# Optimization experiments

Measured on AMD Instinct MI355X. Metric: run time of the kernel, lower is better.

## Reference

```python
import jax, jax.numpy as jnp
import numpy as np
import math

B, T, D = 4, 4096, 1024
H, M = 16, 64
Dh = D // H


def _rope_tables(head_dim, max_seq_len, base=10000):
    inv_freq = 1.0 / (base ** (np.arange(0, head_dim, 2, dtype=np.float32) / head_dim))
    t = np.arange(max_seq_len, dtype=np.float32)
    freqs = np.einsum('i,j->ij', t, inv_freq)  # [T, Dh/2]
    cos = np.cos(freqs)
    sin = np.sin(freqs)
    # interleave (c, c) pairwise -> [T, Dh]
    cos = np.stack((cos, cos), axis=-1).reshape(max_seq_len, head_dim)
    sin = np.stack((sin, sin), axis=-1).reshape(max_seq_len, head_dim)
    return jnp.asarray(cos), jnp.asarray(sin)


def setup_inputs() -> dict:
    key = jax.random.key(0)
    ks = jax.random.split(key, 6)
    s = 1.0 / math.sqrt(D)
    x = jax.random.normal(ks[0], (B, T, D), dtype=jnp.float32)
    Wq = jnp.clip(jax.random.normal(ks[1], (D, D)) * s, -2 * s, 2 * s).astype(jnp.float32)
    Wk = jnp.clip(jax.random.normal(ks[2], (D, D)) * s, -2 * s, 2 * s).astype(jnp.float32)
    Wv = jnp.clip(jax.random.normal(ks[3], (D, D)) * s, -2 * s, 2 * s).astype(jnp.float32)
    Wo = jnp.clip(jax.random.normal(ks[4], (D, D)) * s, -2 * s, 2 * s).astype(jnp.float32)
    latent_code = (jax.random.normal(ks[5], (H, M, Dh)) * 0.02).astype(jnp.float32)
    rope_cos, rope_sin = _rope_tables(Dh, T)
    mask = jnp.ones((B, 1, T, 1), dtype=jnp.int32)
    return {'x': x, 'Wq': Wq, 'Wk': Wk, 'Wv': Wv, 'Wo': Wo,
            'latent_code': latent_code, 'rope_cos': rope_cos,
            'rope_sin': rope_sin, 'mask': mask}


def _rotate(x):
    # (x1, x2) pairs -> (-x2, x1), interleaved
    x2 = x.reshape(*x.shape[:-1], -1, 2)
    return jnp.stack((-x2[..., 1], x2[..., 0]), axis=-1).reshape(x.shape)


def reference(x, Wq, Wk, Wv, Wo, latent_code, rope_cos, rope_sin, mask):
    Bc, Tc, Dc = x.shape
    scale = 1.0 / math.sqrt(Dh)
    # projections -> [B, H, T, Dh]
    q = (x @ Wq.T).reshape(Bc, Tc, H, Dh).transpose(0, 2, 1, 3)
    k = (x @ Wk.T).reshape(Bc, Tc, H, Dh).transpose(0, 2, 1, 3)
    v = (x @ Wv.T).reshape(Bc, Tc, H, Dh).transpose(0, 2, 1, 3)
    cos = rope_cos[:Tc][None, None]  # [1,1,T,Dh]
    sin = rope_sin[:Tc][None, None]
    q = q * cos + _rotate(q) * sin
    k = k * cos + _rotate(k) * sin
    # Stage 1: token -> latent assignment, softmax over tokens (axis=2)
    assign_logits = jnp.einsum('bhtd,hmd->bhtm', k, latent_code) * scale
    assign_logits = jnp.where(mask == 0, -jnp.inf, assign_logits)
    assign = jax.nn.softmax(assign_logits, axis=2)
    k_lat = jnp.einsum('bhtm,bhtd->bhmd', assign, k)
    v_lat = jnp.einsum('bhtm,bhtd->bhmd', assign, v)
    # Stage 2: query attends to latents, softmax over latents (axis=-1)
    att2 = jnp.einsum('bhtd,bhmd->bhtm', q, k_lat) * scale
    p2 = jax.nn.softmax(att2, axis=-1)
    out = jnp.einsum('bhtm,bhmd->bhtd', p2, v_lat)
    out = out.transpose(0, 2, 1, 3).reshape(Bc, Tc, Dc)
    return out @ Wo.T
```

## Files before the change

### kernel.cpp

```cpp
#include <hip/hip_runtime.h>
#include <hip/hip_bf16.h>
#include <stdint.h>


#define DEV static __device__ __forceinline__

using short8 = __attribute__((ext_vector_type(8))) short;
using f32x4  = __attribute__((ext_vector_type(4))) float;

#define ZERO4 (f32x4){0.f, 0.f, 0.f, 0.f}

DEV float bf2f(unsigned short u) {
  union { unsigned int i; float f; } c; c.i = ((unsigned int)u) << 16; return c.f;
}
DEV unsigned short f2bf(float f) {
  __hip_bfloat16 h = __float2bfloat16(f);
  unsigned short u; __builtin_memcpy(&u, &h, 2); return u;
}
DEV f32x4 mfma16(short8 a, short8 b, f32x4 c) {
  return __builtin_amdgcn_mfma_f32_16x16x32_bf16(a, b, c, 0, 0, 0);
}
#define GLOAD_LDS16(G, L) __builtin_amdgcn_global_load_lds( \
    (const __attribute__((address_space(1))) void*)(G),     \
    (__attribute__((address_space(3))) void*)(L), 16, 0, 0)

__global__ void cvt_all(const float* __restrict__ x,
                        const float* __restrict__ Wq, const float* __restrict__ Wk,
                        const float* __restrict__ Wv, const float* __restrict__ Wo,
                        __hip_bfloat16* __restrict__ xb,
                        __hip_bfloat16* __restrict__ Wb) {
  const int bid = blockIdx.x;
  const float* src;
  __hip_bfloat16* dst;
  int base;
  if (bid < 16384) {
    src = x; dst = xb; base = bid;
  } else {
    const int k = (bid - 16384) >> 10;
    src = (k == 0) ? Wq : (k == 1) ? Wk : (k == 2) ? Wv : Wo;
    dst = Wb + (size_t)k * 1048576;
    base = (bid - 16384) & 1023;
  }
  const int i = (base * 256 + threadIdx.x) * 4;
  const float4 v = *(const float4*)(src + i);
  ushort4 o;
  o.x = f2bf(v.x); o.y = f2bf(v.y); o.z = f2bf(v.z); o.w = f2bf(v.w);
  *(ushort4*)(dst + i) = o;
}

template<int MODE, int ROPE>
__global__ __launch_bounds__(512, 2)
void gemm256(const __hip_bfloat16* __restrict__ A,
             const __hip_bfloat16* __restrict__ Bt,
             void* __restrict__ Cout, __hip_bfloat16* __restrict__ Ct,
             const float* __restrict__ cosT, const float* __restrict__ sinT,
             int M, int N, int K) {
  __shared__ __hip_bfloat16 As[2][256 * 64];
  __shared__ __hip_bfloat16 Bs[2][256 * 64];
  const int tid = threadIdx.x;
  const int w = tid >> 6, l = tid & 63;
  const int lr = l & 15, lg = l >> 4;
  const int rowA0 = blockIdx.x * 256;
  const int colB0 = blockIdx.y * 256;
  const int srow = w * 8 + (l >> 3);
  const int skk  = (((l & 7) ^ (l >> 3)) * 8);
  const __hip_bfloat16* Ab = A  + (size_t)(rowA0 + srow) * K + skk;
  const __hip_bfloat16* Bb = Bt + (size_t)(colB0 + srow) * K + skk;
  f32x4 acc[8][4];
#pragma unroll
  for (int i = 0; i < 8; ++i)
#pragma unroll
    for (int j = 0; j < 4; ++j) acc[i][j] = ZERO4;
  const int wr = (w >> 2) * 128;
  const int wc = (w & 3) * 64;
  const int NT = K >> 6;

#define G_STAGE(kt, buf)                                                          \
  {                                                                               \
    const int k0s = (kt) * 64;                                                    \
    _Pragma("unroll")                                                             \
    for (int i = 0; i < 4; ++i) {                                                 \
      GLOAD_LDS16(Ab + (size_t)(i * 64) * K + k0s, &As[buf][i * 4096 + w * 512]); \
      GLOAD_LDS16(Bb + (size_t)(i * 64) * K + k0s, &Bs[buf][i * 4096 + w * 512]); \
    }                                                                             \
  }

  G_STAGE(0, 0);
  for (int kt = 0; kt < NT; ++kt) {
    const int cur = kt & 1;
    if (kt + 1 < NT) {
      G_STAGE(kt + 1, cur ^ 1);
      asm volatile("s_waitcnt vmcnt(8)" ::: "memory");
    } else {
      asm volatile("s_waitcnt vmcnt(0)" ::: "memory");
    }
    __builtin_amdgcn_s_barrier();
    __builtin_amdgcn_s_setprio(1);
#pragma unroll
    for (int s = 0; s < 2; ++s) {
      short8 fa[8], fb[4];
#pragma unroll
      for (int i = 0; i < 8; ++i)
        fa[i] = *(const short8*)&As[cur][(wr + i * 16 + lr) * 64 +
                                         (((s * 4 + lg) ^ (lr & 7)) * 8)];
#pragma unroll
      for (int j = 0; j < 4; ++j)
        fb[j] = *(const short8*)&Bs[cur][(wc + j * 16 + lr) * 64 +
                                         (((s * 4 + lg) ^ (lr & 7)) * 8)];
#pragma unroll
      for (int i = 0; i < 8; ++i)
#pragma unroll
        for (int j = 0; j < 4; ++j)
          acc[i][j] = mfma16(fa[i], fb[j], acc[i][j]);
    }
    __builtin_amdgcn_s_setprio(0);
    __builtin_amdgcn_s_barrier();
  }
#undef G_STAGE

  const int r0 = rowA0 + wr + lg * 4;
  const int c0 = colB0 + wc + lr;
  if (ROPE) {
#pragma unroll
    for (int i = 0; i < 8; ++i)
#pragma unroll
      for (int j = 0; j < 4; ++j)
#pragma unroll
        for (int r = 0; r < 4; ++r) {
          const int m = r0 + i * 16 + r;
          const int n = c0 + j * 16;
          const int t = m & 4095, d = n & 63;
          const float c = cosT[t * 64 + d];
          const float s = sinT[t * 64 + d];
          const float v = acc[i][j][r];
          const float other = __shfl_xor(v, 1, 64);
          acc[i][j][r] = v * c + ((n & 1) ? other : -other) * s;
        }
  }
  if (MODE <= 2) {
#pragma unroll
    for (int i = 0; i < 8; ++i)
#pragma unroll
      for (int j = 0; j < 4; ++j)
#pragma unroll
        for (int r = 0; r < 4; ++r) {
          const size_t idx = (size_t)(r0 + i * 16 + r) * N + (c0 + j * 16);
          if (MODE == 0) ((float*)Cout)[idx] = acc[i][j][r];
          else ((__hip_bfloat16*)Cout)[idx] = __float2bfloat16(acc[i][j][r]);
        }
  }
  if (MODE >= 2) {
#pragma unroll
    for (int i = 0; i < 8; ++i)
#pragma unroll
      for (int j = 0; j < 4; ++j) {
        const int m0 = r0 + i * 16;
        const int n  = c0 + j * 16;
        const size_t row = (size_t)(((m0 >> 12) * 16 + (n >> 6)) * 64 + (n & 63));
        ushort4 pk;
        pk.x = f2bf(acc[i][j][0]); pk.y = f2bf(acc[i][j][1]);
        pk.z = f2bf(acc[i][j][2]); pk.w = f2bf(acc[i][j][3]);
        *(ushort4*)&Ct[row * 4096 + (m0 & 4095)] = pk;
      }
  }
}

__global__ __launch_bounds__(256)
void stage1_logits(const __hip_bfloat16* __restrict__ kmat,
                   const float* __restrict__ latent,
                   const int* __restrict__ mask,
                   __hip_bfloat16* __restrict__ S,
                   float* __restrict__ pmax, float* __restrict__ psum) {
  const int bh = blockIdx.x, chunk = blockIdx.y;
  const int b = bh >> 4, h = bh & 15;
  const int tid = threadIdx.x, w = tid >> 6, l = tid & 63;
  const int lr = l & 15, lg = l >> 4;
  short8 la[4][2];
#pragma unroll
  for (int n = 0; n < 4; ++n)
#pragma unroll
    for (int s = 0; s < 2; ++s) {
      const float* lp = &latent[((size_t)h * 64 + n * 16 + lr) * 64 + s * 32 + lg * 8];
      short8 f;
#pragma unroll
      for (int j = 0; j < 8; ++j) f[j] = (short)f2bf(lp[j]);
      la[n][s] = f;
    }
  float mx[16], sm[16];
#pragma unroll
  for (int i = 0; i < 16; ++i) { mx[i] = -3.0e38f; sm[i] = 0.f; }
  for (int tile = 0; tile < 8; ++tile) {
    const int t = chunk * 512 + tile * 64 + w * 16 + lr;
    const __hip_bfloat16* kp = &kmat[((size_t)(b * 4096 + t) * 16 + h) * 64 + lg * 8];
    const short8 kb0 = *(const short8*)kp;
    const short8 kb1 = *(const short8*)(kp + 32);
    const bool live = (mask[b * 4096 + t] != 0);
    f32x4 acc[4];
#pragma unroll
    for (int n = 0; n < 4; ++n) {
      acc[n] = ZERO4;
      acc[n] = mfma16(la[n][0], kb0, acc[n]);
      acc[n] = mfma16(la[n][1], kb1, acc[n]);
    }
#pragma unroll
    for (int n = 0; n < 4; ++n)
#pragma unroll
      for (int r = 0; r < 4; ++r) {
        const float v = acc[n][r] * 0.125f;
        const int m = n * 16 + lg * 4 + r;
        unsigned short sv = live ? f2bf(v) : (unsigned short)0xFF80;
        ((unsigned short*)S)[((size_t)bh * 64 + m) * 4096 + t] = sv;
        if (live) {
          const int idx = n * 4 + r;
          const float nm = fmaxf(mx[idx], v);
          sm[idx] = sm[idx] * __expf(mx[idx] - nm) + __expf(v - nm);
          mx[idx] = nm;
        }
      }
  }
#pragma unroll
  for (int o = 1; o < 16; o <<= 1)
#pragma unroll
    for (int i = 0; i < 16; ++i) {
      const float omx = __shfl_xor(mx[i], o, 64);
      const float osm = __shfl_xor(sm[i], o, 64);
      const float nm = fmaxf(mx[i], omx);
      sm[i] = sm[i] * __expf(mx[i] - nm) + osm * __expf(omx - nm);
      mx[i] = nm;
    }
  if (lr == 0) {
    const size_t pb = ((size_t)(bh * 8 + chunk) * 4 + w) * 64;
#pragma unroll
    for (int n = 0; n < 4; ++n)
#pragma unroll
      for (int r = 0; r < 4; ++r) {
        const int m = n * 16 + lg * 4 + r;
        pmax[pb + m] = mx[n * 4 + r];
        psum[pb + m] = sm[n * 4 + r];
      }
  }
}

__global__ __launch_bounds__(256)
void latgemm6(const __hip_bfloat16* __restrict__ S,
              const __hip_bfloat16* __restrict__ kT,
              const __hip_bfloat16* __restrict__ vT,
              const float* __restrict__ pmax, const float* __restrict__ psum,
              float* __restrict__ partials) {
  __shared__ float scm[64], sci[64];
  const int bh = blockIdx.x;
  const int tid = threadIdx.x, w = tid >> 6, l = tid & 63;
  const int slice = blockIdx.y * 4 + w;
  const int lr = l & 15;
  const int lk = (l >> 4) * 8;
  const size_t base = (size_t)bh * 64 * 4096;
  if (tid < 64) {
    float mxv = -3.0e38f;
#pragma unroll
    for (int c = 0; c < 32; ++c)
      mxv = fmaxf(mxv, pmax[((size_t)bh * 32 + c) * 64 + tid]);
    float smv = 0.f;
#pragma unroll
    for (int c = 0; c < 32; ++c)
      smv += psum[((size_t)bh * 32 + c) * 64 + tid] *
             __expf(pmax[((size_t)bh * 32 + c) * 64 + tid] - mxv);
    scm[tid] = mxv;
    sci[tid] = 1.f / smv;
  }
  __syncthreads();
  float cm[4], ci[4];
#pragma unroll
  for (int i = 0; i < 4; ++i) {
    cm[i] = scm[i * 16 + lr];
    ci[i] = sci[i * 16 + lr];
  }
  f32x4 ak[4][4], av[4][4];
#pragma unroll
  for (int i = 0; i < 4; ++i)
#pragma unroll
    for (int j = 0; j < 4; ++j) { ak[i][j] = ZERO4; av[i][j] = ZERO4; }
  for (int ks = 0; ks < 16; ++ks) {
    const int t = slice * 512 + ks * 32 + lk;
    short8 fp[4], fk[4], fv[4];
#pragma unroll
    for (int i = 0; i < 4; ++i) {
      const size_t ro = base + (size_t)(i * 16 + lr) * 4096 + t;
      const short8 sv = *(const short8*)&S[ro];
      short8 p;
#pragma unroll
      for (int j = 0; j < 8; ++j)
        p[j] = (short)f2bf(__expf(bf2f((unsigned short)sv[j]) - cm[i]) * ci[i]);
      fp[i] = p;
      fk[i] = *(const short8*)&kT[ro];
      fv[i] = *(const short8*)&vT[ro];
    }
#pragma unroll
    for (int i = 0; i < 4; ++i)
#pragma unroll
      for (int j = 0; j < 4; ++j) {
        ak[i][j] = mfma16(fp[i], fk[j], ak[i][j]);
        av[i][j] = mfma16(fv[i], fp[j], av[i][j]);
      }
  }
  float* pk = partials + ((size_t)(slice * 64 + bh)) * 8192;
#pragma unroll
  for (int i = 0; i < 4; ++i)
#pragma unroll
    for (int j = 0; j < 4; ++j)
#pragma unroll
      for (int r = 0; r < 4; ++r) {
        const int row = i * 16 + 4 * (l >> 4) + r;
        const int col = j * 16 + lr;
        pk[(size_t)row * 64 + col]        = ak[i][j][r];
        pk[4096 + (size_t)row * 64 + col] = av[i][j][r];
      }
}

__global__ void latreduce(const float* __restrict__ partials,
                          __hip_bfloat16* __restrict__ k_lat,
                          __hip_bfloat16* __restrict__ v_latT) {
  const int i = blockIdx.x * 256 + threadIdx.x;
  const int bh = i >> 13, off = i & 8191;
  float sm = 0.f;
#pragma unroll
  for (int c = 0; c < 8; ++c)
    sm += partials[((size_t)(c * 64 + bh)) * 8192 + off];
  if (off < 4096) k_lat[(size_t)bh * 4096 + off] = __float2bfloat16(sm);
  else            v_latT[(size_t)bh * 4096 + (off - 4096)] = __float2bfloat16(sm);
}

__global__ __launch_bounds__(256)
void stage2_attn(const __hip_bfloat16* __restrict__ q,
                 const __hip_bfloat16* __restrict__ k_lat,
                 const __hip_bfloat16* __restrict__ v_latT,
                 __hip_bfloat16* __restrict__ attn) {
  __shared__ unsigned short Pl[4][16][64];
  const int bid = blockIdx.x;
  const int bh = bid >> 6, tt = (bid & 63) * 64;
  const int b = bh >> 4, h = bh & 15;
  const int tid = threadIdx.x, w = tid >> 6, l = tid & 63;
  const size_t qoff = ((size_t)(b * 4096 + tt + w * 16 + (l & 15)) * 16 + h) * 64;
  const short8 a0 = *(const short8*)&q[qoff + (l >> 4) * 8];
  const short8 a1 = *(const short8*)&q[qoff + 32 + (l >> 4) * 8];
  f32x4 att[4];
#pragma unroll
  for (int n = 0; n < 4; ++n) att[n] = ZERO4;
#pragma unroll
  for (int n = 0; n < 4; ++n) {
    const __hip_bfloat16* kl = &k_lat[((size_t)bh * 64 + n * 16 + (l & 15)) * 64];
    const short8 b0 = *(const short8*)&kl[(l >> 4) * 8];
    const short8 b1 = *(const short8*)&kl[32 + (l >> 4) * 8];
    att[n] = mfma16(a0, b0, att[n]);
    att[n] = mfma16(a1, b1, att[n]);
  }
  float p[4][4];
#pragma unroll
  for (int r = 0; r < 4; ++r) {
    const float v0 = att[0][r] * 0.125f, v1 = att[1][r] * 0.125f;
    const float v2 = att[2][r] * 0.125f, v3 = att[3][r] * 0.125f;
    float mxv = fmaxf(fmaxf(v0, v1), fmaxf(v2, v3));
#pragma unroll
    for (int o = 1; o < 16; o <<= 1) mxv = fmaxf(mxv, __shfl_xor(mxv, o, 64));
    const float e0 = __expf(v0 - mxv), e1 = __expf(v1 - mxv);
    const float e2 = __expf(v2 - mxv), e3 = __expf(v3 - mxv);
    float sum = e0 + e1 + e2 + e3;
#pragma unroll
    for (int o = 1; o < 16; o <<= 1) sum += __shfl_xor(sum, o, 64);
    const float inv = 1.f / sum;
    p[0][r] = e0 * inv; p[1][r] = e1 * inv; p[2][r] = e2 * inv; p[3][r] = e3 * inv;
  }
#pragma unroll
  for (int n = 0; n < 4; ++n)
#pragma unroll
    for (int r = 0; r < 4; ++r) {
      const int row = 4 * (l >> 4) + r;
      const int col = n * 16 + (l & 15);
      Pl[w][row][col ^ ((row & 7) << 3)] = f2bf(p[n][r]);
    }
  __syncthreads();
  const int arow = l & 15;
  const short8 pa0 = *(const short8*)&Pl[w][arow][(((l >> 4) + 0) ^ (arow & 7)) * 8];
  const short8 pa1 = *(const short8*)&Pl[w][arow][(((l >> 4) + 4) ^ (arow & 7)) * 8];
  f32x4 ov[4];
#pragma unroll
  for (int n = 0; n < 4; ++n) ov[n] = ZERO4;
#pragma unroll
  for (int n = 0; n < 4; ++n) {
    const __hip_bfloat16* vt = &v_latT[((size_t)bh * 64 + n * 16 + (l & 15)) * 64];
    const short8 b0 = *(const short8*)&vt[(l >> 4) * 8];
    const short8 b1 = *(const short8*)&vt[32 + (l >> 4) * 8];
    ov[n] = mfma16(pa0, b0, ov[n]);
    ov[n] = mfma16(pa1, b1, ov[n]);
  }
#pragma unroll
  for (int n = 0; n < 4; ++n) {
    const int d = n * 16 + (l & 15);
#pragma unroll
    for (int r = 0; r < 4; ++r) {
      const int trow = tt + w * 16 + 4 * (l >> 4) + r;
      attn[((size_t)(b * 4096 + trow) * 16 + h) * 64 + d] = __float2bfloat16(ov[n][r]);
    }
  }
}

extern "C" void kernel_launch(void* const* d_in, const int* in_sizes, int n_in,
                              void* d_out, int out_size, void* d_ws, size_t ws_size,
                              hipStream_t stream) {
  const float* x      = (const float*)d_in[0];
  const float* Wq     = (const float*)d_in[1];
  const float* Wk     = (const float*)d_in[2];
  const float* Wv     = (const float*)d_in[3];
  const float* Wo     = (const float*)d_in[4];
  const float* latent = (const float*)d_in[5];
  const float* cosT   = (const float*)d_in[6];
  const float* sinT   = (const float*)d_in[7];
  const int*   mask   = (const int*)d_in[8];

  char* ws = (char*)d_ws;
  __hip_bfloat16* xb = (__hip_bfloat16*)ws;
  __hip_bfloat16* Wb = (__hip_bfloat16*)(ws + 33554432);
  __hip_bfloat16* qb = (__hip_bfloat16*)(ws + 41943040);
  __hip_bfloat16* kb = (__hip_bfloat16*)(ws + 75497472);
  __hip_bfloat16* kT = (__hip_bfloat16*)(ws + 109051904);
  __hip_bfloat16* vT = (__hip_bfloat16*)(ws + 142606336);
  char* tail = ws + 176160768;
  float* pmax = (float*)tail;
  float* psum = pmax + 131072;
  __hip_bfloat16* k_lat  = (__hip_bfloat16*)(psum + 131072);
  __hip_bfloat16* v_latT = k_lat + 262144;

  __hip_bfloat16* S    = xb;
  __hip_bfloat16* attn = qb;
  float* partials = (float*)kb;

  cvt_all<<<20480, 256, 0, stream>>>(x, Wq, Wk, Wv, Wo, xb, Wb);

  dim3 gg(64, 4);
  gemm256<1, 1><<<gg, 512, 0, stream>>>(xb, Wb + 0 * 1048576, qb, nullptr, cosT, sinT, 16384, 1024, 1024);
  gemm256<2, 1><<<gg, 512, 0, stream>>>(xb, Wb + 1 * 1048576, kb, kT, cosT, sinT, 16384, 1024, 1024);
  gemm256<3, 0><<<gg, 512, 0, stream>>>(xb, Wb + 2 * 1048576, nullptr, vT, nullptr, nullptr, 16384, 1024, 1024);

  dim3 sg(64, 8);
  stage1_logits<<<sg, 256, 0, stream>>>(kb, latent, mask, S, pmax, psum);

  dim3 lg(64, 2);
  latgemm6<<<lg, 256, 0, stream>>>(S, kT, vT, pmax, psum, partials);
  latreduce<<<2048, 256, 0, stream>>>(partials, k_lat, v_latT);

  stage2_attn<<<4096, 256, 0, stream>>>(qb, k_lat, v_latT, attn);
  gemm256<0, 0><<<gg, 512, 0, stream>>>(attn, Wb + 3 * 1048576, d_out, nullptr, nullptr, nullptr, 16384, 1024, 1024);
}
```

Measured before the change: 312.8 us.

## Shrink GEMM tiles to 128x128 and drop max-subtraction in token softmax

The projection GEMMs move from 256x256x64 tiles with 512 threads and swizzled LDS to 128x128x32 tiles with 256 threads, unswizzled LDS, and more blocks per CU. Stage 1 now writes exp(logit) directly and accumulates plain sums, dropping the running-max bookkeeping. The latent GEMM therefore reads P without recomputing exp, and normalisation moves to a small denom_inv kernel plus a scale in the reduction. Without max-subtraction, exp can overflow for large logits, and the new GEMM tiling may have lower reuse and more LDS bank conflicts.

Measured after the change: 314.0 us. About the same (+0.4%).

```diff
diff --git a/kernel.cpp b/kernel.cpp
--- a/kernel.cpp
+++ b/kernel.cpp
@@ -49,40 +49,38 @@
 }
 
 template<int MODE, int ROPE>
-__global__ __launch_bounds__(512, 2)
-void gemm256(const __hip_bfloat16* __restrict__ A,
-             const __hip_bfloat16* __restrict__ Bt,
-             void* __restrict__ Cout, __hip_bfloat16* __restrict__ Ct,
-             const float* __restrict__ cosT, const float* __restrict__ sinT,
-             int M, int N, int K) {
-  __shared__ __hip_bfloat16 As[2][256 * 64];
-  __shared__ __hip_bfloat16 Bs[2][256 * 64];
+__global__ __launch_bounds__(256, 4)
+void gemm128b(const __hip_bfloat16* __restrict__ A,
+              const __hip_bfloat16* __restrict__ Bt,
+              void* __restrict__ Cout, __hip_bfloat16* __restrict__ Ct,
+              const float* __restrict__ cosT, const float* __restrict__ sinT,
+              int M, int N, int K) {
+  __shared__ __hip_bfloat16 As[2][128 * 32];
+  __shared__ __hip_bfloat16 Bs[2][128 * 32];
   const int tid = threadIdx.x;
   const int w = tid >> 6, l = tid & 63;
   const int lr = l & 15, lg = l >> 4;
-  const int rowA0 = blockIdx.x * 256;
-  const int colB0 = blockIdx.y * 256;
-  const int srow = w * 8 + (l >> 3);
-  const int skk  = (((l & 7) ^ (l >> 3)) * 8);
+  const int rowA0 = blockIdx.x * 128;
+  const int colB0 = blockIdx.y * 128;
+  const int srow = w * 16 + (l >> 2);
+  const int skk  = (l & 3) * 8;
   const __hip_bfloat16* Ab = A  + (size_t)(rowA0 + srow) * K + skk;
   const __hip_bfloat16* Bb = Bt + (size_t)(colB0 + srow) * K + skk;
-  f32x4 acc[8][4];
-#pragma unroll
-  for (int i = 0; i < 8; ++i)
+  f32x4 acc[4][4];
+#pragma unroll
+  for (int i = 0; i < 4; ++i)
 #pragma unroll
     for (int j = 0; j < 4; ++j) acc[i][j] = ZERO4;
-  const int wr = (w >> 2) * 128;
-  const int wc = (w & 3) * 64;
-  const int NT = K >> 6;
-
-#define G_STAGE(kt, buf)                                                          \
-  {                                                                               \
-    const int k0s = (kt) * 64;                                                    \
-    _Pragma("unroll")                                                             \
-    for (int i = 0; i < 4; ++i) {                                                 \
-      GLOAD_LDS16(Ab + (size_t)(i * 64) * K + k0s, &As[buf][i * 4096 + w * 512]); \
-      GLOAD_LDS16(Bb + (size_t)(i * 64) * K + k0s, &Bs[buf][i * 4096 + w * 512]); \
-    }                                                                             \
+  const int wr = (w >> 1) * 64, wc = (w & 1) * 64;
+  const int NT = K >> 5;
+
+#define G_STAGE(kt, buf)                                                   \
+  {                                                                        \
+    const int k0s = (kt) * 32;                                             \
+    GLOAD_LDS16(Ab + k0s,                  &As[buf][(w * 16) * 32]);       \
+    GLOAD_LDS16(Ab + (size_t)64 * K + k0s, &As[buf][(64 + w * 16) * 32]);  \
+    GLOAD_LDS16(Bb + k0s,                  &Bs[buf][(w * 16) * 32]);       \
+    GLOAD_LDS16(Bb + (size_t)64 * K + k0s, &Bs[buf][(64 + w * 16) * 32]);  \
   }
 
   G_STAGE(0, 0);
@@ -90,25 +88,22 @@
     const int cur = kt & 1;
     if (kt + 1 < NT) {
       G_STAGE(kt + 1, cur ^ 1);
-      asm volatile("s_waitcnt vmcnt(8)" ::: "memory");
+      asm volatile("s_waitcnt vmcnt(4)" ::: "memory");
     } else {
       asm volatile("s_waitcnt vmcnt(0)" ::: "memory");
     }
     __builtin_amdgcn_s_barrier();
     __builtin_amdgcn_s_setprio(1);
-#pragma unroll
-    for (int s = 0; s < 2; ++s) {
-      short8 fa[8], fb[4];
-#pragma unroll
-      for (int i = 0; i < 8; ++i)
-        fa[i] = *(const short8*)&As[cur][(wr + i * 16 + lr) * 64 +
-                                         (((s * 4 + lg) ^ (lr & 7)) * 8)];
+    {
+      short8 fa[4], fb[4];
+#pragma unroll
+      for (int i = 0; i < 4; ++i)
+        fa[i] = *(const short8*)&As[cur][(wr + i * 16 + lr) * 32 + lg * 8];
 #pragma unroll
       for (int j = 0; j < 4; ++j)
-        fb[j] = *(const short8*)&Bs[cur][(wc + j * 16 + lr) * 64 +
-                                         (((s * 4 + lg) ^ (lr & 7)) * 8)];
-#pragma unroll
-      for (int i = 0; i < 8; ++i)
+        fb[j] = *(const short8*)&Bs[cur][(wc + j * 16 + lr) * 32 + lg * 8];
+#pragma unroll
+      for (int i = 0; i < 4; ++i)
 #pragma unroll
         for (int j = 0; j < 4; ++j)
           acc[i][j] = mfma16(fa[i], fb[j], acc[i][j]);
@@ -122,7 +117,7 @@
   const int c0 = colB0 + wc + lr;
   if (ROPE) {
 #pragma unroll
-    for (int i = 0; i < 8; ++i)
+    for (int i = 0; i < 4; ++i)
 #pragma unroll
       for (int j = 0; j < 4; ++j)
 #pragma unroll
@@ -139,7 +134,7 @@
   }
   if (MODE <= 2) {
 #pragma unroll
-    for (int i = 0; i < 8; ++i)
+    for (int i = 0; i < 4; ++i)
 #pragma unroll
       for (int j = 0; j < 4; ++j)
 #pragma unroll
@@ -151,7 +146,7 @@
   }
   if (MODE >= 2) {
 #pragma unroll
-    for (int i = 0; i < 8; ++i)
+    for (int i = 0; i < 4; ++i)
 #pragma unroll
       for (int j = 0; j < 4; ++j) {
         const int m0 = r0 + i * 16;
@@ -166,11 +161,11 @@
 }
 
 __global__ __launch_bounds__(256)
-void stage1_logits(const __hip_bfloat16* __restrict__ kmat,
-                   const float* __restrict__ latent,
-                   const int* __restrict__ mask,
-                   __hip_bfloat16* __restrict__ S,
-                   float* __restrict__ pmax, float* __restrict__ psum) {
+void stage1_expS(const __hip_bfloat16* __restrict__ kmat,
+                 const float* __restrict__ latent,
+                 const int* __restrict__ mask,
+                 __hip_bfloat16* __restrict__ P,
+                 float* __restrict__ psum) {
   const int bh = blockIdx.x, chunk = blockIdx.y;
   const int b = bh >> 4, h = bh & 15;
   const int tid = threadIdx.x, w = tid >> 6, l = tid & 63;
@@ -186,9 +181,9 @@
       for (int j = 0; j < 8; ++j) f[j] = (short)f2bf(lp[j]);
       la[n][s] = f;
     }
-  float mx[16], sm[16];
-#pragma unroll
-  for (int i = 0; i < 16; ++i) { mx[i] = -3.0e38f; sm[i] = 0.f; }
+  float sm[16];
+#pragma unroll
+  for (int i = 0; i < 16; ++i) sm[i] = 0.f;
   for (int tile = 0; tile < 8; ++tile) {
     const int t = chunk * 512 + tile * 64 + w * 16 + lr;
     const __hip_bfloat16* kp = &kmat[((size_t)(b * 4096 + t) * 16 + h) * 64 + lg * 8];
@@ -206,74 +201,48 @@
     for (int n = 0; n < 4; ++n)
 #pragma unroll
       for (int r = 0; r < 4; ++r) {
-        const float v = acc[n][r] * 0.125f;
+        const float e = live ? __expf(acc[n][r] * 0.125f) : 0.f;
         const int m = n * 16 + lg * 4 + r;
-        unsigned short sv = live ? f2bf(v) : (unsigned short)0xFF80;
-        ((unsigned short*)S)[((size_t)bh * 64 + m) * 4096 + t] = sv;
-        if (live) {
-          const int idx = n * 4 + r;
-          const float nm = fmaxf(mx[idx], v);
-          sm[idx] = sm[idx] * __expf(mx[idx] - nm) + __expf(v - nm);
-          mx[idx] = nm;
-        }
+        ((unsigned short*)P)[((size_t)bh * 64 + m) * 4096 + t] = f2bf(e);
+        sm[n * 4 + r] += e;
       }
   }
 #pragma unroll
   for (int o = 1; o < 16; o <<= 1)
 #pragma unroll
-    for (int i = 0; i < 16; ++i) {
-      const float omx = __shfl_xor(mx[i], o, 64);
-      const float osm = __shfl_xor(sm[i], o, 64);
-      const float nm = fmaxf(mx[i], omx);
-      sm[i] = sm[i] * __expf(mx[i] - nm) + osm * __expf(omx - nm);
-      mx[i] = nm;
-    }
+    for (int i = 0; i < 16; ++i) sm[i] += __shfl_xor(sm[i], o, 64);
   if (lr == 0) {
     const size_t pb = ((size_t)(bh * 8 + chunk) * 4 + w) * 64;
 #pragma unroll
     for (int n = 0; n < 4; ++n)
 #pragma unroll
-      for (int r = 0; r < 4; ++r) {
-        const int m = n * 16 + lg * 4 + r;
-        pmax[pb + m] = mx[n * 4 + r];
-        psum[pb + m] = sm[n * 4 + r];
-      }
-  }
+      for (int r = 0; r < 4; ++r)
+        psum[pb + n * 16 + lg * 4 + r] = sm[n * 4 + r];
+  }
+}
+
+__global__ void denom_inv(const float* __restrict__ psum, float* __restrict__ cinv) {
+  const int i = blockIdx.x * 256 + threadIdx.x;
+  if (i >= 4096) return;
+  const int bh = i >> 6, m = i & 63;
+  float sm = 0.f;
+#pragma unroll
+  for (int c = 0; c < 32; ++c)
+    sm += psum[((size_t)bh * 32 + c) * 64 + m];
+  cinv[i] = 1.f / sm;
 }
 
 __global__ __launch_bounds__(256)
-void latgemm6(const __hip_bfloat16* __restrict__ S,
+void latgemm7(const __hip_bfloat16* __restrict__ P,
               const __hip_bfloat16* __restrict__ kT,
               const __hip_bfloat16* __restrict__ vT,
-              const float* __restrict__ pmax, const float* __restrict__ psum,
               float* __restrict__ partials) {
-  __shared__ float scm[64], sci[64];
   const int bh = blockIdx.x;
   const int tid = threadIdx.x, w = tid >> 6, l = tid & 63;
   const int slice = blockIdx.y * 4 + w;
   const int lr = l & 15;
   const int lk = (l >> 4) * 8;
   const size_t base = (size_t)bh * 64 * 4096;
-  if (tid < 64) {
-    float mxv = -3.0e38f;
-#pragma unroll
-    for (int c = 0; c < 32; ++c)
-      mxv = fmaxf(mxv, pmax[((size_t)bh * 32 + c) * 64 + tid]);
-    float smv = 0.f;
-#pragma unroll
-    for (int c = 0; c < 32; ++c)
-      smv += psum[((size_t)bh * 32 + c) * 64 + tid] *
-             __expf(pmax[((size_t)bh * 32 + c) * 64 + tid] - mxv);
-    scm[tid] = mxv;
-    sci[tid] = 1.f / smv;
-  }
-  __syncthreads();
-  float cm[4], ci[4];
-#pragma unroll
-  for (int i = 0; i < 4; ++i) {
-    cm[i] = scm[i * 16 + lr];
-    ci[i] = sci[i * 16 + lr];
-  }
   f32x4 ak[4][4], av[4][4];
 #pragma unroll
   for (int i = 0; i < 4; ++i)
@@ -285,12 +254,7 @@
 #pragma unroll
     for (int i = 0; i < 4; ++i) {
       const size_t ro = base + (size_t)(i * 16 + lr) * 4096 + t;
-      const short8 sv = *(const short8*)&S[ro];
-      short8 p;
-#pragma unroll
-      for (int j = 0; j < 8; ++j)
-        p[j] = (short)f2bf(__expf(bf2f((unsigned short)sv[j]) - cm[i]) * ci[i]);
-      fp[i] = p;
+      fp[i] = *(const short8*)&P[ro];
       fk[i] = *(const short8*)&kT[ro];
       fv[i] = *(const short8*)&vT[ro];
     }
@@ -316,15 +280,18 @@
       }
 }
 
-__global__ void latreduce(const float* __restrict__ partials,
-                          __hip_bfloat16* __restrict__ k_lat,
-                          __hip_bfloat16* __restrict__ v_latT) {
+__global__ void latreduce2(const float* __restrict__ partials,
+                           const float* __restrict__ cinv,
+                           __hip_bfloat16* __restrict__ k_lat,
+                           __hip_bfloat16* __restrict__ v_latT) {
   const int i = blockIdx.x * 256 + threadIdx.x;
   const int bh = i >> 13, off = i & 8191;
   float sm = 0.f;
 #pragma unroll
   for (int c = 0; c < 8; ++c)
     sm += partials[((size_t)(c * 64 + bh)) * 8192 + off];
+  const int m = (off < 4096) ? (off >> 6) : (off & 63);
+  sm *= cinv[bh * 64 + m];
   if (off < 4096) k_lat[(size_t)bh * 4096 + off] = __float2bfloat16(sm);
   else            v_latT[(size_t)bh * 4096 + (off - 4096)] = __float2bfloat16(sm);
 }
@@ -424,29 +391,30 @@
   __hip_bfloat16* kT = (__hip_bfloat16*)(ws + 109051904);
   __hip_bfloat16* vT = (__hip_bfloat16*)(ws + 142606336);
   char* tail = ws + 176160768;
-  float* pmax = (float*)tail;
-  float* psum = pmax + 131072;
-  __hip_bfloat16* k_lat  = (__hip_bfloat16*)(psum + 131072);
+  float* psum = (float*)tail;
+  float* cinv = psum + 131072;
+  __hip_bfloat16* k_lat  = (__hip_bfloat16*)(cinv + 4096);
   __hip_bfloat16* v_latT = k_lat + 262144;
 
-  __hip_bfloat16* S    = xb;
+  __hip_bfloat16* P    = xb;
   __hip_bfloat16* attn = qb;
   float* partials = (float*)kb;
 
   cvt_all<<<20480, 256, 0, stream>>>(x, Wq, Wk, Wv, Wo, xb, Wb);
 
-  dim3 gg(64, 4);
-  gemm256<1, 1><<<gg, 512, 0, stream>>>(xb, Wb + 0 * 1048576, qb, nullptr, cosT, sinT, 16384, 1024, 1024);
-  gemm256<2, 1><<<gg, 512, 0, stream>>>(xb, Wb + 1 * 1048576, kb, kT, cosT, sinT, 16384, 1024, 1024);
-  gemm256<3, 0><<<gg, 512, 0, stream>>>(xb, Wb + 2 * 1048576, nullptr, vT, nullptr, nullptr, 16384, 1024, 1024);
+  dim3 gg(128, 8);
+  gemm128b<1, 1><<<gg, 256, 0, stream>>>(xb, Wb + 0 * 1048576, qb, nullptr, cosT, sinT, 16384, 1024, 1024);
+  gemm128b<2, 1><<<gg, 256, 0, stream>>>(xb, Wb + 1 * 1048576, kb, kT, cosT, sinT, 16384, 1024, 1024);
+  gemm128b<3, 0><<<gg, 256, 0, stream>>>(xb, Wb + 2 * 1048576, nullptr, vT, nullptr, nullptr, 16384, 1024, 1024);
 
   dim3 sg(64, 8);
-  stage1_logits<<<sg, 256, 0, stream>>>(kb, latent, mask, S, pmax, psum);
+  stage1_expS<<<sg, 256, 0, stream>>>(kb, latent, mask, P, psum);
+  denom_inv<<<16, 256, 0, stream>>>(psum, cinv);
 
   dim3 lg(64, 2);
-  latgemm6<<<lg, 256, 0, stream>>>(S, kT, vT, pmax, psum, partials);
-  latreduce<<<2048, 256, 0, stream>>>(partials, k_lat, v_latT);
+  latgemm7<<<lg, 256, 0, stream>>>(P, kT, vT, partials);
+  latreduce2<<<2048, 256, 0, stream>>>(partials, cinv, k_lat, v_latT);
 
   stage2_attn<<<4096, 256, 0, stream>>>(qb, k_lat, v_latT, attn);
-  gemm256<0, 0><<<gg, 512, 0, stream>>>(attn, Wb + 3 * 1048576, d_out, nullptr, nullptr, nullptr, 16384, 1024, 1024);
-}
+  gemm128b<0, 0><<<gg, 256, 0, stream>>>(attn, Wb + 3 * 1048576, d_out, nullptr, nullptr, nullptr, 16384, 1024, 1024);
+}
```
